# Optimization experiments

Measured on AMD Instinct MI355X. Metric: run time of the kernel, lower is better.

The kernel has to match this reference:

```python
import jax, jax.numpy as jnp
import numpy as np
import math

B, T, C = 2, 2048, 1024
H = 16
D = C // H  # 64


def setup_inputs() -> dict:
    key = jax.random.key(0)
    ks = jax.random.split(key, 12)
    s = 1.0 / math.sqrt(C)
    inp = {
        "q": jax.random.normal(ks[0], (B, T, C), dtype=jnp.float32),
        "k": jax.random.normal(ks[1], (B, T, C), dtype=jnp.float32),
        "v": jax.random.normal(ks[2], (B, T, C), dtype=jnp.float32),
        # causal mask, broadcastable to [B, H, T, T]; 0 -> masked
        "mask": jnp.tril(jnp.ones((T, T), dtype=jnp.int32))[None, None, :, :],
        "Wq": jax.random.normal(ks[3], (C, C), dtype=jnp.float32) * s,
        "bq": jnp.zeros((C,), dtype=jnp.float32),
        "Wk": jax.random.normal(ks[4], (C, C), dtype=jnp.float32) * s,
        "bk": jnp.zeros((C,), dtype=jnp.float32),
        "Wv": jax.random.normal(ks[5], (C, C), dtype=jnp.float32) * s,
        "bv": jnp.zeros((C,), dtype=jnp.float32),
        "Wo": jax.random.normal(ks[6], (C, C), dtype=jnp.float32) * s,
        "bo": jnp.zeros((C,), dtype=jnp.float32),
    }
    return inp


def reference(q, k, v, mask, Wq, bq, Wk, bk, Wv, bv, Wo, bo):
    # Linear projections (torch Linear: x @ W.T + b), split into heads -> [B,H,T,D]
    qh = (q @ Wq.T + bq).reshape(B, T, H, D).transpose(0, 2, 1, 3)
    kh = (k @ Wk.T + bk).reshape(B, T, H, D).transpose(0, 2, 1, 3)
    vh = (v @ Wv.T + bv).reshape(B, T, H, D).transpose(0, 2, 1, 3)
    # scaled dot-product attention with full [B,H,T,T] scores (faithful to source)
    scores = jnp.einsum("bhqd,bhkd->bhqk", qh, kh) / math.sqrt(D)
    scores = jnp.where(mask == 0, -jnp.inf, scores)
    attn = jax.nn.softmax(scores, axis=-1)  # dropout = identity (eval mode)
    out = jnp.einsum("bhqk,bhkd->bhqd", attn, vh)
    out = out.transpose(0, 2, 1, 3).reshape(B, T, C)
    return out @ Wo.T + bo
```

## Files before the change

kernel.cpp:

```cpp
#include <hip/hip_runtime.h>
#include <hip/hip_bf16.h>
#include <cstdint>
#include <cstddef>

#define B_ 2
#define T_ 2048
#define C_ 1024
#define H_ 16
#define D_ 64

typedef unsigned short u16;
typedef unsigned int u32;

typedef __bf16 bf16x8 __attribute__((ext_vector_type(8)));
typedef float f32x4 __attribute__((ext_vector_type(4)));

union BFQ {
    uint4 q;
    bf16x8 v;
    u16 s[8];
};

__device__ __forceinline__ u16 f2bf(float f) {
    union { float f; u32 u; } x;
    x.f = f;
    u32 u = x.u;
    return (u16)((u + 0x7FFFu + ((u >> 16) & 1u)) >> 16);
}

__device__ __forceinline__ void gl_lds16(const u16* g, u16* l) {
    __builtin_amdgcn_global_load_lds(
        (const __attribute__((address_space(1))) u32*)g,
        (__attribute__((address_space(3))) u32*)l, 16, 0, 0);
}

__global__ void cvt3_kernel(const float* __restrict__ i0, const float* __restrict__ i1,
                            const float* __restrict__ i2, u16* __restrict__ o0,
                            u16* __restrict__ o1, u16* __restrict__ o2, int n4) {
    const float* in = blockIdx.z == 0 ? i0 : (blockIdx.z == 1 ? i1 : i2);
    u16* out = blockIdx.z == 0 ? o0 : (blockIdx.z == 1 ? o1 : o2);
    int i = blockIdx.x * blockDim.x + threadIdx.x;
    int stride = gridDim.x * blockDim.x;
    for (; i < n4; i += stride) {
        float4 f = reinterpret_cast<const float4*>(in)[i];
        ushort4 o;
        o.x = f2bf(f.x);
        o.y = f2bf(f.y);
        o.z = f2bf(f.z);
        o.w = f2bf(f.w);
        reinterpret_cast<ushort4*>(out)[i] = o;
    }
}

__global__ void cvt4_kernel(const float* __restrict__ i0, const float* __restrict__ i1,
                            const float* __restrict__ i2, const float* __restrict__ i3,
                            u16* __restrict__ o0, u16* __restrict__ o1,
                            u16* __restrict__ o2, u16* __restrict__ o3, int n4) {
    int z = blockIdx.z;
    const float* in = z == 0 ? i0 : (z == 1 ? i1 : (z == 2 ? i2 : i3));
    u16* out = z == 0 ? o0 : (z == 1 ? o1 : (z == 2 ? o2 : o3));
    int i = blockIdx.x * blockDim.x + threadIdx.x;
    int stride = gridDim.x * blockDim.x;
    for (; i < n4; i += stride) {
        float4 f = reinterpret_cast<const float4*>(in)[i];
        ushort4 o;
        o.x = f2bf(f.x);
        o.y = f2bf(f.y);
        o.z = f2bf(f.z);
        o.w = f2bf(f.w);
        reinterpret_cast<ushort4*>(out)[i] = o;
    }
}

template <int OUT_BF16>
__device__ __forceinline__ void gemm_body(const u16* __restrict__ A,
                                          const u16* __restrict__ Bw,
                                          const float* __restrict__ bias,
                                          void* __restrict__ Cout,
                                          int M, int N, int K) {
    __shared__ u16 As[2][128 * 64];
    __shared__ u16 Bs[2][64 * 64];

    const int tid = threadIdx.x;
    const int lane = tid & 63;
    const int wave = tid >> 6;
    const int wm = wave >> 1, wn = wave & 1;
    const int g = lane >> 4, r = lane & 15;
    const int m0 = blockIdx.y * 128, n0 = blockIdx.x * 64;

    f32x4 acc[4][2] = {};

    const int lrow = lane >> 3;
    const int lcolS = ((lane & 7) ^ (lane >> 3)) * 8;
    const u16* Abase = A + (size_t)(m0 + lrow) * K + lcolS;
    const u16* Bbase = Bw + (size_t)(n0 + lrow) * K + lcolS;

#pragma unroll
    for (int c = 0; c < 4; ++c) {
        int ca = 4 * wave + c;
        gl_lds16(Abase + (size_t)(8 * ca) * K, As[0] + ca * 512);
    }
#pragma unroll
    for (int c = 0; c < 2; ++c) {
        int cb = 2 * wave + c;
        gl_lds16(Bbase + (size_t)(8 * cb) * K, Bs[0] + cb * 512);
    }
    __syncthreads();

    int cur = 0;
    for (int k0 = 0; k0 < K; k0 += 64) {
        if (k0 + 64 < K) {
#pragma unroll
            for (int c = 0; c < 4; ++c) {
                int ca = 4 * wave + c;
                gl_lds16(Abase + (size_t)(8 * ca) * K + k0 + 64, As[cur ^ 1] + ca * 512);
            }
#pragma unroll
            for (int c = 0; c < 2; ++c) {
                int cb = 2 * wave + c;
                gl_lds16(Bbase + (size_t)(8 * cb) * K + k0 + 64, Bs[cur ^ 1] + cb * 512);
            }
        }

#pragma unroll
        for (int kk = 0; kk < 2; ++kk) {
            bf16x8 af[4], bfv[2];
#pragma unroll
            for (int mt = 0; mt < 4; ++mt) {
                int row = wm * 64 + mt * 16 + r;
                BFQ u;
                u.q = *(const uint4*)(As[cur] + row * 64 + (((kk * 4 + g) ^ (r & 7)) * 8));
                af[mt] = u.v;
            }
#pragma unroll
            for (int nt = 0; nt < 2; ++nt) {
                int row = wn * 32 + nt * 16 + r;
                BFQ u;
                u.q = *(const uint4*)(Bs[cur] + row * 64 + (((kk * 4 + g) ^ (r & 7)) * 8));
                bfv[nt] = u.v;
            }
            __builtin_amdgcn_s_setprio(1);
#pragma unroll
            for (int mt = 0; mt < 4; ++mt)
#pragma unroll
                for (int nt = 0; nt < 2; ++nt)
                    acc[mt][nt] = __builtin_amdgcn_mfma_f32_16x16x32_bf16(af[mt], bfv[nt], acc[mt][nt], 0, 0, 0);
            __builtin_amdgcn_s_setprio(0);
        }
        __syncthreads();
        cur ^= 1;
    }

#pragma unroll
    for (int mt = 0; mt < 4; ++mt) {
#pragma unroll
        for (int nt = 0; nt < 2; ++nt) {
            int n = n0 + wn * 32 + nt * 16 + r;
            float bv = bias[n];
#pragma unroll
            for (int j = 0; j < 4; ++j) {
                int m = m0 + wm * 64 + mt * 16 + g * 4 + j;
                float val = acc[mt][nt][j] + bv;
                if (OUT_BF16)
                    ((u16*)Cout)[(size_t)m * N + n] = f2bf(val);
                else
                    ((float*)Cout)[(size_t)m * N + n] = val;
            }
        }
    }
}

__global__ __launch_bounds__(256, 2) void gemm3_kernel(
    const u16* __restrict__ A0, const u16* __restrict__ A1, const u16* __restrict__ A2,
    const u16* __restrict__ W0, const u16* __restrict__ W1, const u16* __restrict__ W2,
    const float* __restrict__ b0, const float* __restrict__ b1, const float* __restrict__ b2,
    u16* __restrict__ C0, u16* __restrict__ C1, u16* __restrict__ C2,
    int M, int N, int K) {
    int z = blockIdx.z;
    const u16* A = z == 0 ? A0 : (z == 1 ? A1 : A2);
    const u16* W = z == 0 ? W0 : (z == 1 ? W1 : W2);
    const float* bias = z == 0 ? b0 : (z == 1 ? b1 : b2);
    u16* C = z == 0 ? C0 : (z == 1 ? C1 : C2);
    gemm_body<1>(A, W, bias, C, M, N, K);
}

__global__ __launch_bounds__(256, 2) void gemm_f32_kernel(const u16* __restrict__ A,
                                                          const u16* __restrict__ W,
                                                          const float* __restrict__ bias,
                                                          float* __restrict__ C,
                                                          int M, int N, int K) {
    gemm_body<0>(A, W, bias, C, M, N, K);
}


__device__ __forceinline__ void softmax_step(f32x4* s, int domask, int kv0, int qrow0,
                                             int g, int r, float* m_run, float* l_run,
                                             f32x4* o_acc, u16* pl) {
    float sv[4][4];
#pragma unroll
    for (int nt = 0; nt < 4; ++nt) {
#pragma unroll
        for (int j = 0; j < 4; ++j) {
            float x = s[nt][j] * 0.125f;
            if (domask) {
                int kg = kv0 + nt * 16 + r;
                int qg = qrow0 + g * 4 + j;
                x = (kg <= qg) ? x : -1e30f;
            }
            sv[nt][j] = x;
        }
    }
    float rm[4];
#pragma unroll
    for (int j = 0; j < 4; ++j) {
        float m = fmaxf(fmaxf(sv[0][j], sv[1][j]), fmaxf(sv[2][j], sv[3][j]));
        m = fmaxf(m, __shfl_xor(m, 1));
        m = fmaxf(m, __shfl_xor(m, 2));
        m = fmaxf(m, __shfl_xor(m, 4));
        m = fmaxf(m, __shfl_xor(m, 8));
        rm[j] = m;
    }
    float grow = fmaxf(fmaxf(rm[0] - m_run[0], rm[1] - m_run[1]),
                       fmaxf(rm[2] - m_run[2], rm[3] - m_run[3]));
    float pout[4][4];
    float rs[4];
    if (__all(grow <= 8.0f)) {
#pragma unroll
        for (int j = 0; j < 4; ++j) {
            float mref = m_run[j];
            float p0 = __expf(sv[0][j] - mref);
            float p1 = __expf(sv[1][j] - mref);
            float p2 = __expf(sv[2][j] - mref);
            float p3 = __expf(sv[3][j] - mref);
            pout[0][j] = p0; pout[1][j] = p1; pout[2][j] = p2; pout[3][j] = p3;
            rs[j] = (p0 + p1) + (p2 + p3);
        }
    } else {
#pragma unroll
        for (int j = 0; j < 4; ++j) {
            float mnew = fmaxf(m_run[j], rm[j]);
            float fac = __expf(m_run[j] - mnew);
            float p0 = __expf(sv[0][j] - mnew);
            float p1 = __expf(sv[1][j] - mnew);
            float p2 = __expf(sv[2][j] - mnew);
            float p3 = __expf(sv[3][j] - mnew);
            pout[0][j] = p0; pout[1][j] = p1; pout[2][j] = p2; pout[3][j] = p3;
            rs[j] = (p0 + p1) + (p2 + p3);
            l_run[j] *= fac;
            m_run[j] = mnew;
#pragma unroll
            for (int nt = 0; nt < 4; ++nt) o_acc[nt][j] *= fac;
        }
    }
#pragma unroll
    for (int j = 0; j < 4; ++j) {
        float t = rs[j];
        t += __shfl_xor(t, 1);
        t += __shfl_xor(t, 2);
        t += __shfl_xor(t, 4);
        t += __shfl_xor(t, 8);
        l_run[j] += t;
        int q = g * 4 + j;
        int sw = (q & 7) << 3;
        pl[(q * 64 + 0 * 16 + r) ^ sw] = f2bf(pout[0][j]);
        pl[(q * 64 + 1 * 16 + r) ^ sw] = f2bf(pout[1][j]);
        pl[(q * 64 + 2 * 16 + r) ^ sw] = f2bf(pout[2][j]);
        pl[(q * 64 + 3 * 16 + r) ^ sw] = f2bf(pout[3][j]);
    }
}

__global__ __launch_bounds__(256, 2) void attn_kernel(const u16* __restrict__ Qp,
                                                      const u16* __restrict__ Kp,
                                                      const u16* __restrict__ Vp,
                                                      u16* __restrict__ Op) {
    __shared__ u16 Vt[64 * 64];
    __shared__ u16 Pl[4][2][16 * 64];

    const int tid = threadIdx.x, lane = tid & 63, wave = tid >> 6;
    const int g = lane >> 4, r = lane & 15;
    const int bh = blockIdx.y, b = bh >> 4, h = bh & 15;
    const int i = blockIdx.x;
    const int qA0 = i * 64;
    const int qB0 = (31 - i) * 64;

    const u16* Qbh = Qp + ((size_t)b * T_) * C_ + h * 64;
    const u16* Kbh = Kp + ((size_t)b * T_) * C_ + h * 64;
    const u16* Vbh = Vp + ((size_t)b * T_) * C_ + h * 64;
    u16* Obh = Op + ((size_t)b * T_) * C_ + h * 64;

    bf16x8 aqA[2], aqB[2];
    {
        const u16* qa = Qbh + (size_t)(qA0 + wave * 16 + r) * C_ + g * 8;
        const u16* qb = Qbh + (size_t)(qB0 + wave * 16 + r) * C_ + g * 8;
        BFQ u0, u1, u2, u3;
        u0.q = *(const uint4*)(qa);
        u1.q = *(const uint4*)(qa + 32);
        u2.q = *(const uint4*)(qb);
        u3.q = *(const uint4*)(qb + 32);
        aqA[0] = u0.v; aqA[1] = u1.v;
        aqB[0] = u2.v; aqB[1] = u3.v;
    }

    float mA[4], lA[4], mB[4], lB[4];
    f32x4 oA[4] = {}, oB[4] = {};
#pragma unroll
    for (int j = 0; j < 4; ++j) {
        mA[j] = -1e30f; lA[j] = 0.f;
        mB[j] = -1e30f; lB[j] = 0.f;
    }

    const int vp = tid & 31;
    const int vd0 = (tid >> 5) * 8;

    BFQ kf[2][4];
#pragma unroll
    for (int kk = 0; kk < 2; ++kk)
#pragma unroll
        for (int nt = 0; nt < 4; ++nt)
            kf[kk][nt].q = *(const uint4*)(Kbh + (size_t)(nt * 16 + r) * C_ + kk * 32 + g * 8);
    BFQ va, vb;
    {
        const u16* vr0 = Vbh + (size_t)(2 * vp) * C_ + vd0;
        va.q = *(const uint4*)(vr0);
        vb.q = *(const uint4*)(vr0 + C_);
    }

    for (int kv0 = 0; kv0 <= qB0; kv0 += 64) {
        const int actA = (kv0 <= qA0);

        __builtin_amdgcn_s_barrier();

#pragma unroll
        for (int ii = 0; ii < 8; ++ii) {
            int d = vd0 + ii;
            u32 pr = (u32)va.s[ii] | ((u32)vb.s[ii] << 16);
            *(u32*)&Vt[(d * 64 + 2 * vp) ^ ((d & 7) << 3)] = pr;
        }

        f32x4 sB[4] = {}, sA[4] = {};
        __builtin_amdgcn_s_setprio(1);
#pragma unroll
        for (int kk = 0; kk < 2; ++kk)
#pragma unroll
            for (int nt = 0; nt < 4; ++nt)
                sB[nt] = __builtin_amdgcn_mfma_f32_16x16x32_bf16(aqB[kk], kf[kk][nt].v, sB[nt], 0, 0, 0);
        if (actA) {
#pragma unroll
            for (int kk = 0; kk < 2; ++kk)
#pragma unroll
                for (int nt = 0; nt < 4; ++nt)
                    sA[nt] = __builtin_amdgcn_mfma_f32_16x16x32_bf16(aqA[kk], kf[kk][nt].v, sA[nt], 0, 0, 0);
        }
        __builtin_amdgcn_s_setprio(0);

        if (kv0 + 64 <= qB0) {
            const u16* kn = Kbh + (size_t)(kv0 + 64) * C_;
#pragma unroll
            for (int kk = 0; kk < 2; ++kk)
#pragma unroll
                for (int nt = 0; nt < 4; ++nt)
                    kf[kk][nt].q = *(const uint4*)(kn + (size_t)(nt * 16 + r) * C_ + kk * 32 + g * 8);
            const u16* vr0 = Vbh + (size_t)(kv0 + 64 + 2 * vp) * C_ + vd0;
            va.q = *(const uint4*)(vr0);
            vb.q = *(const uint4*)(vr0 + C_);
        }

        softmax_step(sB, kv0 == qB0, kv0, qB0 + wave * 16, g, r, mB, lB, oB, Pl[wave][0]);
        if (actA)
            softmax_step(sA, kv0 == qA0, kv0, qA0 + wave * 16, g, r, mA, lA, oA, Pl[wave][1]);

        asm volatile("s_waitcnt lgkmcnt(0)" ::: "memory");
        __builtin_amdgcn_s_barrier();

        bf16x8 vf[2][4];
#pragma unroll
        for (int kk = 0; kk < 2; ++kk)
#pragma unroll
            for (int nt = 0; nt < 4; ++nt) {
                int d = nt * 16 + r;
                BFQ u;
                u.q = *(const uint4*)&Vt[(d * 64 + kk * 32 + g * 8) ^ ((d & 7) << 3)];
                vf[kk][nt] = u.v;
            }

        __builtin_amdgcn_s_setprio(1);
#pragma unroll
        for (int kk = 0; kk < 2; ++kk) {
            BFQ ua;
            ua.q = *(const uint4*)&Pl[wave][0][(r * 64 + kk * 32 + g * 8) ^ ((r & 7) << 3)];
#pragma unroll
            for (int nt = 0; nt < 4; ++nt)
                oB[nt] = __builtin_amdgcn_mfma_f32_16x16x32_bf16(ua.v, vf[kk][nt], oB[nt], 0, 0, 0);
        }
        if (actA) {
#pragma unroll
            for (int kk = 0; kk < 2; ++kk) {
                BFQ ua;
                ua.q = *(const uint4*)&Pl[wave][1][(r * 64 + kk * 32 + g * 8) ^ ((r & 7) << 3)];
#pragma unroll
                for (int nt = 0; nt < 4; ++nt)
                    oA[nt] = __builtin_amdgcn_mfma_f32_16x16x32_bf16(ua.v, vf[kk][nt], oA[nt], 0, 0, 0);
            }
        }
        __builtin_amdgcn_s_setprio(0);
    }

#pragma unroll
    for (int nt = 0; nt < 4; ++nt) {
#pragma unroll
        for (int j = 0; j < 4; ++j) {
            int qgB = qB0 + wave * 16 + g * 4 + j;
            Obh[(size_t)qgB * C_ + nt * 16 + r] = f2bf(oB[nt][j] / lB[j]);
            int qgA = qA0 + wave * 16 + g * 4 + j;
            Obh[(size_t)qgA * C_ + nt * 16 + r] = f2bf(oA[nt][j] / lA[j]);
        }
    }
}

extern "C" void kernel_launch(void* const* d_in, const int* in_sizes, int n_in,
                              void* d_out, int out_size, void* d_ws, size_t ws_size,
                              hipStream_t stream) {
    const float* q = (const float*)d_in[0];
    const float* k = (const float*)d_in[1];
    const float* v = (const float*)d_in[2];
    const float* Wq = (const float*)d_in[4];
    const float* bq = (const float*)d_in[5];
    const float* Wk = (const float*)d_in[6];
    const float* bk = (const float*)d_in[7];
    const float* Wv = (const float*)d_in[8];
    const float* bv = (const float*)d_in[9];
    const float* Wo = (const float*)d_in[10];
    const float* bo = (const float*)d_in[11];

    const size_t NTC = (size_t)B_ * T_ * C_;
    const size_t NW = (size_t)C_ * C_;

    char* ws = (char*)d_ws;
    size_t off = 0;
    u16* qb = (u16*)(ws + off);  off += NTC * 2;
    u16* kb = (u16*)(ws + off);  off += NTC * 2;
    u16* vb = (u16*)(ws + off);  off += NTC * 2;
    u16* Wqb = (u16*)(ws + off); off += NW * 2;
    u16* Wkb = (u16*)(ws + off); off += NW * 2;
    u16* Wvb = (u16*)(ws + off); off += NW * 2;
    u16* Wob = (u16*)(ws + off); off += NW * 2;
    u16* Qp = (u16*)(ws + off);  off += NTC * 2;
    u16* Kp = (u16*)(ws + off);  off += NTC * 2;
    u16* Vp = (u16*)(ws + off);  off += NTC * 2;
    u16* AOb = (u16*)(ws + off); off += NTC * 2;

    cvt3_kernel<<<dim3(512, 1, 3), 256, 0, stream>>>(q, k, v, qb, kb, vb, (int)(NTC / 4));
    cvt4_kernel<<<dim3(128, 1, 4), 256, 0, stream>>>(Wq, Wk, Wv, Wo, Wqb, Wkb, Wvb, Wob, (int)(NW / 4));

    const int M = B_ * T_;
    dim3 g3(C_ / 64, M / 128, 3);
    gemm3_kernel<<<g3, 256, 0, stream>>>(qb, kb, vb, Wqb, Wkb, Wvb, bq, bk, bv,
                                         Qp, Kp, Vp, M, C_, C_);

    dim3 agrid(16, B_ * H_);
    attn_kernel<<<agrid, 256, 0, stream>>>(Qp, Kp, Vp, AOb);

    dim3 g1(C_ / 64, M / 128, 1);
    gemm_f32_kernel<<<g1, 256, 0, stream>>>(AOb, Wob, bo, (float*)d_out, M, C_, C_);
}
```

Before: 157.7 us.

## Split attention tiles across 8 waves and fold softmax scale into Q with exp2

The attention block grows to 512 threads. Waves 0-3 handle the late (long) query tile and waves 4-7 handle the early tile, so each wave keeps one set of accumulators instead of two, which lowers register pressure and adds parallelism. Q is pre-scaled by log2(e)/sqrt(D) so softmax can use the hardware exp2 directly, with the deferred-rescale threshold adjusted to match. The GEMM launch bounds are raised to 3 blocks per CU, and float-to-bf16 conversion now uses the native cast. The risks are that the early-tile waves sit idle once their tile is done yet still join the barriers, and that rounding the scaled Q to bf16 adds a little error.

Measured after the change: 196.0 us. 1.24x slower.

```diff
diff --git a/kernel.cpp b/kernel.cpp
--- a/kernel.cpp
+++ b/kernel.cpp
@@ -15,17 +15,25 @@
 typedef __bf16 bf16x8 __attribute__((ext_vector_type(8)));
 typedef float f32x4 __attribute__((ext_vector_type(4)));
 
+#define QSCALE 0.18033688011112042f
+#define DEFER_THR 11.5f
+
 union BFQ {
     uint4 q;
     bf16x8 v;
     u16 s[8];
 };
 
+__device__ __forceinline__ float bf2f(u16 s) {
+    union { u32 u; float f; } x;
+    x.u = ((u32)s) << 16;
+    return x.f;
+}
+
 __device__ __forceinline__ u16 f2bf(float f) {
-    union { float f; u32 u; } x;
-    x.f = f;
-    u32 u = x.u;
-    return (u16)((u + 0x7FFFu + ((u >> 16) & 1u)) >> 16);
+    union { __bf16 h; u16 u; } c;
+    c.h = (__bf16)f;
+    return c.u;
 }
 
 __device__ __forceinline__ void gl_lds16(const u16* g, u16* l) {
@@ -170,7 +178,7 @@
     }
 }
 
-__global__ __launch_bounds__(256, 2) void gemm3_kernel(
+__global__ __launch_bounds__(256, 3) void gemm3_kernel(
     const u16* __restrict__ A0, const u16* __restrict__ A1, const u16* __restrict__ A2,
     const u16* __restrict__ W0, const u16* __restrict__ W1, const u16* __restrict__ W2,
     const float* __restrict__ b0, const float* __restrict__ b1, const float* __restrict__ b2,
@@ -184,7 +192,7 @@
     gemm_body<1>(A, W, bias, C, M, N, K);
 }
 
-__global__ __launch_bounds__(256, 2) void gemm_f32_kernel(const u16* __restrict__ A,
+__global__ __launch_bounds__(256, 3) void gemm_f32_kernel(const u16* __restrict__ A,
                                                           const u16* __restrict__ W,
                                                           const float* __restrict__ bias,
                                                           float* __restrict__ C,
@@ -201,7 +209,7 @@
     for (int nt = 0; nt < 4; ++nt) {
 #pragma unroll
         for (int j = 0; j < 4; ++j) {
-            float x = s[nt][j] * 0.125f;
+            float x = s[nt][j];
             if (domask) {
                 int kg = kv0 + nt * 16 + r;
                 int qg = qrow0 + g * 4 + j;
@@ -224,14 +232,14 @@
                        fmaxf(rm[2] - m_run[2], rm[3] - m_run[3]));
     float pout[4][4];
     float rs[4];
-    if (__all(grow <= 8.0f)) {
+    if (__all(grow <= DEFER_THR)) {
 #pragma unroll
         for (int j = 0; j < 4; ++j) {
             float mref = m_run[j];
-            float p0 = __expf(sv[0][j] - mref);
-            float p1 = __expf(sv[1][j] - mref);
-            float p2 = __expf(sv[2][j] - mref);
-            float p3 = __expf(sv[3][j] - mref);
+            float p0 = __builtin_amdgcn_exp2f(sv[0][j] - mref);
+            float p1 = __builtin_amdgcn_exp2f(sv[1][j] - mref);
+            float p2 = __builtin_amdgcn_exp2f(sv[2][j] - mref);
+            float p3 = __builtin_amdgcn_exp2f(sv[3][j] - mref);
             pout[0][j] = p0; pout[1][j] = p1; pout[2][j] = p2; pout[3][j] = p3;
             rs[j] = (p0 + p1) + (p2 + p3);
         }
@@ -239,11 +247,11 @@
 #pragma unroll
         for (int j = 0; j < 4; ++j) {
             float mnew = fmaxf(m_run[j], rm[j]);
-            float fac = __expf(m_run[j] - mnew);
-            float p0 = __expf(sv[0][j] - mnew);
-            float p1 = __expf(sv[1][j] - mnew);
-            float p2 = __expf(sv[2][j] - mnew);
-            float p3 = __expf(sv[3][j] - mnew);
+            float fac = __builtin_amdgcn_exp2f(m_run[j] - mnew);
+            float p0 = __builtin_amdgcn_exp2f(sv[0][j] - mnew);
+            float p1 = __builtin_amdgcn_exp2f(sv[1][j] - mnew);
+            float p2 = __builtin_amdgcn_exp2f(sv[2][j] - mnew);
+            float p3 = __builtin_amdgcn_exp2f(sv[3][j] - mnew);
             pout[0][j] = p0; pout[1][j] = p1; pout[2][j] = p2; pout[3][j] = p3;
             rs[j] = (p0 + p1) + (p2 + p3);
             l_run[j] *= fac;
@@ -269,48 +277,54 @@
     }
 }
 
-__global__ __launch_bounds__(256, 2) void attn_kernel(const u16* __restrict__ Qp,
+__global__ __launch_bounds__(512, 2) void attn_kernel(const u16* __restrict__ Qp,
                                                       const u16* __restrict__ Kp,
                                                       const u16* __restrict__ Vp,
                                                       u16* __restrict__ Op) {
     __shared__ u16 Vt[64 * 64];
-    __shared__ u16 Pl[4][2][16 * 64];
+    __shared__ u16 Pl[8][16 * 64];
 
     const int tid = threadIdx.x, lane = tid & 63, wave = tid >> 6;
     const int g = lane >> 4, r = lane & 15;
+    const int tileSel = wave >> 2;
+    const int wsub = wave & 3;
     const int bh = blockIdx.y, b = bh >> 4, h = bh & 15;
     const int i = blockIdx.x;
-    const int qA0 = i * 64;
     const int qB0 = (31 - i) * 64;
+    const int q0 = tileSel ? i * 64 : qB0;
 
     const u16* Qbh = Qp + ((size_t)b * T_) * C_ + h * 64;
     const u16* Kbh = Kp + ((size_t)b * T_) * C_ + h * 64;
     const u16* Vbh = Vp + ((size_t)b * T_) * C_ + h * 64;
     u16* Obh = Op + ((size_t)b * T_) * C_ + h * 64;
 
-    bf16x8 aqA[2], aqB[2];
+    bf16x8 aq[2];
     {
-        const u16* qa = Qbh + (size_t)(qA0 + wave * 16 + r) * C_ + g * 8;
-        const u16* qb = Qbh + (size_t)(qB0 + wave * 16 + r) * C_ + g * 8;
-        BFQ u0, u1, u2, u3;
+        const u16* qa = Qbh + (size_t)(q0 + wsub * 16 + r) * C_ + g * 8;
+        BFQ u0, u1;
         u0.q = *(const uint4*)(qa);
         u1.q = *(const uint4*)(qa + 32);
-        u2.q = *(const uint4*)(qb);
-        u3.q = *(const uint4*)(qb + 32);
-        aqA[0] = u0.v; aqA[1] = u1.v;
-        aqB[0] = u2.v; aqB[1] = u3.v;
-    }
-
-    float mA[4], lA[4], mB[4], lB[4];
-    f32x4 oA[4] = {}, oB[4] = {};
+#pragma unroll
+        for (int e = 0; e < 8; ++e) {
+            u0.s[e] = f2bf(bf2f(u0.s[e]) * QSCALE);
+            u1.s[e] = f2bf(bf2f(u1.s[e]) * QSCALE);
+        }
+        aq[0] = u0.v;
+        aq[1] = u1.v;
+    }
+
+    float m_run[4], l_run[4];
+    f32x4 o_acc[4] = {};
 #pragma unroll
     for (int j = 0; j < 4; ++j) {
-        mA[j] = -1e30f; lA[j] = 0.f;
-        mB[j] = -1e30f; lB[j] = 0.f;
-    }
-
-    const int vp = tid & 31;
-    const int vd0 = (tid >> 5) * 8;
+        m_run[j] = -1e30f;
+        l_run[j] = 0.f;
+    }
+
+    const int stager = tileSel;
+    const int st = tid & 255;
+    const int vp = st & 31;
+    const int vd0 = (st >> 5) * 8;
 
     BFQ kf[2][4];
 #pragma unroll
@@ -319,100 +333,87 @@
         for (int nt = 0; nt < 4; ++nt)
             kf[kk][nt].q = *(const uint4*)(Kbh + (size_t)(nt * 16 + r) * C_ + kk * 32 + g * 8);
     BFQ va, vb;
-    {
+    if (stager) {
         const u16* vr0 = Vbh + (size_t)(2 * vp) * C_ + vd0;
         va.q = *(const uint4*)(vr0);
         vb.q = *(const uint4*)(vr0 + C_);
     }
 
     for (int kv0 = 0; kv0 <= qB0; kv0 += 64) {
-        const int actA = (kv0 <= qA0);
+        const int act = (kv0 <= q0);
 
         __builtin_amdgcn_s_barrier();
 
-#pragma unroll
-        for (int ii = 0; ii < 8; ++ii) {
-            int d = vd0 + ii;
-            u32 pr = (u32)va.s[ii] | ((u32)vb.s[ii] << 16);
-            *(u32*)&Vt[(d * 64 + 2 * vp) ^ ((d & 7) << 3)] = pr;
-        }
-
-        f32x4 sB[4] = {}, sA[4] = {};
-        __builtin_amdgcn_s_setprio(1);
-#pragma unroll
-        for (int kk = 0; kk < 2; ++kk)
-#pragma unroll
-            for (int nt = 0; nt < 4; ++nt)
-                sB[nt] = __builtin_amdgcn_mfma_f32_16x16x32_bf16(aqB[kk], kf[kk][nt].v, sB[nt], 0, 0, 0);
-        if (actA) {
+        if (stager) {
+#pragma unroll
+            for (int ii = 0; ii < 8; ++ii) {
+                int d = vd0 + ii;
+                u32 pr = (u32)va.s[ii] | ((u32)vb.s[ii] << 16);
+                *(u32*)&Vt[(d * 64 + 2 * vp) ^ ((d & 7) << 3)] = pr;
+            }
+        }
+
+        f32x4 s[4] = {};
+        if (act) {
+            __builtin_amdgcn_s_setprio(1);
 #pragma unroll
             for (int kk = 0; kk < 2; ++kk)
 #pragma unroll
                 for (int nt = 0; nt < 4; ++nt)
-                    sA[nt] = __builtin_amdgcn_mfma_f32_16x16x32_bf16(aqA[kk], kf[kk][nt].v, sA[nt], 0, 0, 0);
-        }
-        __builtin_amdgcn_s_setprio(0);
-
-        if (kv0 + 64 <= qB0) {
+                    s[nt] = __builtin_amdgcn_mfma_f32_16x16x32_bf16(aq[kk], kf[kk][nt].v, s[nt], 0, 0, 0);
+            __builtin_amdgcn_s_setprio(0);
+        }
+
+        if (kv0 + 64 <= q0) {
             const u16* kn = Kbh + (size_t)(kv0 + 64) * C_;
 #pragma unroll
             for (int kk = 0; kk < 2; ++kk)
 #pragma unroll
                 for (int nt = 0; nt < 4; ++nt)
                     kf[kk][nt].q = *(const uint4*)(kn + (size_t)(nt * 16 + r) * C_ + kk * 32 + g * 8);
+        }
+        if (stager && kv0 + 64 <= qB0) {
             const u16* vr0 = Vbh + (size_t)(kv0 + 64 + 2 * vp) * C_ + vd0;
             va.q = *(const uint4*)(vr0);
             vb.q = *(const uint4*)(vr0 + C_);
         }
 
-        softmax_step(sB, kv0 == qB0, kv0, qB0 + wave * 16, g, r, mB, lB, oB, Pl[wave][0]);
-        if (actA)
-            softmax_step(sA, kv0 == qA0, kv0, qA0 + wave * 16, g, r, mA, lA, oA, Pl[wave][1]);
+        if (act)
+            softmax_step(s, kv0 == q0, kv0, q0 + wsub * 16, g, r, m_run, l_run, o_acc, Pl[wave]);
 
         asm volatile("s_waitcnt lgkmcnt(0)" ::: "memory");
         __builtin_amdgcn_s_barrier();
 
-        bf16x8 vf[2][4];
-#pragma unroll
-        for (int kk = 0; kk < 2; ++kk)
-#pragma unroll
-            for (int nt = 0; nt < 4; ++nt) {
-                int d = nt * 16 + r;
-                BFQ u;
-                u.q = *(const uint4*)&Vt[(d * 64 + kk * 32 + g * 8) ^ ((d & 7) << 3)];
-                vf[kk][nt] = u.v;
-            }
-
-        __builtin_amdgcn_s_setprio(1);
-#pragma unroll
-        for (int kk = 0; kk < 2; ++kk) {
-            BFQ ua;
-            ua.q = *(const uint4*)&Pl[wave][0][(r * 64 + kk * 32 + g * 8) ^ ((r & 7) << 3)];
-#pragma unroll
-            for (int nt = 0; nt < 4; ++nt)
-                oB[nt] = __builtin_amdgcn_mfma_f32_16x16x32_bf16(ua.v, vf[kk][nt], oB[nt], 0, 0, 0);
-        }
-        if (actA) {
+        if (act) {
+            bf16x8 vf[2][4];
+#pragma unroll
+            for (int kk = 0; kk < 2; ++kk)
+#pragma unroll
+                for (int nt = 0; nt < 4; ++nt) {
+                    int d = nt * 16 + r;
+                    BFQ u;
+                    u.q = *(const uint4*)&Vt[(d * 64 + kk * 32 + g * 8) ^ ((d & 7) << 3)];
+                    vf[kk][nt] = u.v;
+                }
+            __builtin_amdgcn_s_setprio(1);
 #pragma unroll
             for (int kk = 0; kk < 2; ++kk) {
                 BFQ ua;
-                ua.q = *(const uint4*)&Pl[wave][1][(r * 64 + kk * 32 + g * 8) ^ ((r & 7) << 3)];
+                ua.q = *(const uint4*)&Pl[wave][(r * 64 + kk * 32 + g * 8) ^ ((r & 7) << 3)];
 #pragma unroll
                 for (int nt = 0; nt < 4; ++nt)
-                    oA[nt] = __builtin_amdgcn_mfma_f32_16x16x32_bf16(ua.v, vf[kk][nt], oA[nt], 0, 0, 0);
-            }
-        }
-        __builtin_amdgcn_s_setprio(0);
+                    o_acc[nt] = __builtin_amdgcn_mfma_f32_16x16x32_bf16(ua.v, vf[kk][nt], o_acc[nt], 0, 0, 0);
+            }
+            __builtin_amdgcn_s_setprio(0);
+        }
     }
 
 #pragma unroll
     for (int nt = 0; nt < 4; ++nt) {
 #pragma unroll
         for (int j = 0; j < 4; ++j) {
-            int qgB = qB0 + wave * 16 + g * 4 + j;
-            Obh[(size_t)qgB * C_ + nt * 16 + r] = f2bf(oB[nt][j] / lB[j]);
-            int qgA = qA0 + wave * 16 + g * 4 + j;
-            Obh[(size_t)qgA * C_ + nt * 16 + r] = f2bf(oA[nt][j] / lA[j]);
+            int qg = q0 + wsub * 16 + g * 4 + j;
+            Obh[(size_t)qg * C_ + nt * 16 + r] = f2bf(o_acc[nt][j] / l_run[j]);
         }
     }
 }
@@ -458,7 +459,7 @@
                                          Qp, Kp, Vp, M, C_, C_);
 
     dim3 agrid(16, B_ * H_);
-    attn_kernel<<<agrid, 256, 0, stream>>>(Qp, Kp, Vp, AOb);
+    attn_kernel<<<agrid, 512, 0, stream>>>(Qp, Kp, Vp, AOb);
 
     dim3 g1(C_ / 64, M / 128, 1);
     gemm_f32_kernel<<<g1, 256, 0, stream>>>(AOb, Wob, bo, (float*)d_out, M, C_, C_);
```

## Split attention KV loop across two blocks and merge partial softmax results

Applied to the files above, without the earlier changes.

The attention grid doubles along z. Each block handles alternating 64-key tiles and writes unnormalized bf16 partial outputs plus running max and sum, and a new merge kernel combines the two halves with log-sum-exp weights. The goal is more parallelism from 512 attention blocks instead of 256. Q is also prescaled by log2(e)/sqrt(D) so the softmax can use exp2 directly, with a looser deferred-rescale threshold, and the GEMM launch bounds move to 3 blocks per CU. In exchange the unnormalized partials are rounded to bf16, and the merge kernel adds a launch plus extra global traffic.

Measured after the change: 168.7 us. +7.0%, slower.

```diff
diff --git a/kernel.cpp b/kernel.cpp
--- a/kernel.cpp
+++ b/kernel.cpp
@@ -15,17 +15,25 @@
 typedef __bf16 bf16x8 __attribute__((ext_vector_type(8)));
 typedef float f32x4 __attribute__((ext_vector_type(4)));
 
+#define QSCALE 0.18033688011112042f
+#define DEFER_THR 11.5f
+
 union BFQ {
     uint4 q;
     bf16x8 v;
     u16 s[8];
 };
 
+__device__ __forceinline__ float bf2f(u16 s) {
+    union { u32 u; float f; } x;
+    x.u = ((u32)s) << 16;
+    return x.f;
+}
+
 __device__ __forceinline__ u16 f2bf(float f) {
-    union { float f; u32 u; } x;
-    x.f = f;
-    u32 u = x.u;
-    return (u16)((u + 0x7FFFu + ((u >> 16) & 1u)) >> 16);
+    union { __bf16 h; u16 u; } c;
+    c.h = (__bf16)f;
+    return c.u;
 }
 
 __device__ __forceinline__ void gl_lds16(const u16* g, u16* l) {
@@ -170,7 +178,7 @@
     }
 }
 
-__global__ __launch_bounds__(256, 2) void gemm3_kernel(
+__global__ __launch_bounds__(256, 3) void gemm3_kernel(
     const u16* __restrict__ A0, const u16* __restrict__ A1, const u16* __restrict__ A2,
     const u16* __restrict__ W0, const u16* __restrict__ W1, const u16* __restrict__ W2,
     const float* __restrict__ b0, const float* __restrict__ b1, const float* __restrict__ b2,
@@ -184,7 +192,7 @@
     gemm_body<1>(A, W, bias, C, M, N, K);
 }
 
-__global__ __launch_bounds__(256, 2) void gemm_f32_kernel(const u16* __restrict__ A,
+__global__ __launch_bounds__(256, 3) void gemm_f32_kernel(const u16* __restrict__ A,
                                                           const u16* __restrict__ W,
                                                           const float* __restrict__ bias,
                                                           float* __restrict__ C,
@@ -201,7 +209,7 @@
     for (int nt = 0; nt < 4; ++nt) {
 #pragma unroll
         for (int j = 0; j < 4; ++j) {
-            float x = s[nt][j] * 0.125f;
+            float x = s[nt][j];
             if (domask) {
                 int kg = kv0 + nt * 16 + r;
                 int qg = qrow0 + g * 4 + j;
@@ -224,14 +232,14 @@
                        fmaxf(rm[2] - m_run[2], rm[3] - m_run[3]));
     float pout[4][4];
     float rs[4];
-    if (__all(grow <= 8.0f)) {
+    if (__all(grow <= DEFER_THR)) {
 #pragma unroll
         for (int j = 0; j < 4; ++j) {
             float mref = m_run[j];
-            float p0 = __expf(sv[0][j] - mref);
-            float p1 = __expf(sv[1][j] - mref);
-            float p2 = __expf(sv[2][j] - mref);
-            float p3 = __expf(sv[3][j] - mref);
+            float p0 = __builtin_amdgcn_exp2f(sv[0][j] - mref);
+            float p1 = __builtin_amdgcn_exp2f(sv[1][j] - mref);
+            float p2 = __builtin_amdgcn_exp2f(sv[2][j] - mref);
+            float p3 = __builtin_amdgcn_exp2f(sv[3][j] - mref);
             pout[0][j] = p0; pout[1][j] = p1; pout[2][j] = p2; pout[3][j] = p3;
             rs[j] = (p0 + p1) + (p2 + p3);
         }
@@ -239,11 +247,11 @@
 #pragma unroll
         for (int j = 0; j < 4; ++j) {
             float mnew = fmaxf(m_run[j], rm[j]);
-            float fac = __expf(m_run[j] - mnew);
-            float p0 = __expf(sv[0][j] - mnew);
-            float p1 = __expf(sv[1][j] - mnew);
-            float p2 = __expf(sv[2][j] - mnew);
-            float p3 = __expf(sv[3][j] - mnew);
+            float fac = __builtin_amdgcn_exp2f(m_run[j] - mnew);
+            float p0 = __builtin_amdgcn_exp2f(sv[0][j] - mnew);
+            float p1 = __builtin_amdgcn_exp2f(sv[1][j] - mnew);
+            float p2 = __builtin_amdgcn_exp2f(sv[2][j] - mnew);
+            float p3 = __builtin_amdgcn_exp2f(sv[3][j] - mnew);
             pout[0][j] = p0; pout[1][j] = p1; pout[2][j] = p2; pout[3][j] = p3;
             rs[j] = (p0 + p1) + (p2 + p3);
             l_run[j] *= fac;
@@ -272,7 +280,9 @@
 __global__ __launch_bounds__(256, 2) void attn_kernel(const u16* __restrict__ Qp,
                                                       const u16* __restrict__ Kp,
                                                       const u16* __restrict__ Vp,
-                                                      u16* __restrict__ Op) {
+                                                      u16* __restrict__ OP0,
+                                                      u16* __restrict__ OP1,
+                                                      float* __restrict__ ML) {
     __shared__ u16 Vt[64 * 64];
     __shared__ u16 Pl[4][2][16 * 64];
 
@@ -280,13 +290,13 @@
     const int g = lane >> 4, r = lane & 15;
     const int bh = blockIdx.y, b = bh >> 4, h = bh & 15;
     const int i = blockIdx.x;
+    const int z = blockIdx.z;
     const int qA0 = i * 64;
     const int qB0 = (31 - i) * 64;
 
     const u16* Qbh = Qp + ((size_t)b * T_) * C_ + h * 64;
     const u16* Kbh = Kp + ((size_t)b * T_) * C_ + h * 64;
     const u16* Vbh = Vp + ((size_t)b * T_) * C_ + h * 64;
-    u16* Obh = Op + ((size_t)b * T_) * C_ + h * 64;
 
     bf16x8 aqA[2], aqB[2];
     {
@@ -297,6 +307,13 @@
         u1.q = *(const uint4*)(qa + 32);
         u2.q = *(const uint4*)(qb);
         u3.q = *(const uint4*)(qb + 32);
+#pragma unroll
+        for (int e = 0; e < 8; ++e) {
+            u0.s[e] = f2bf(bf2f(u0.s[e]) * QSCALE);
+            u1.s[e] = f2bf(bf2f(u1.s[e]) * QSCALE);
+            u2.s[e] = f2bf(bf2f(u2.s[e]) * QSCALE);
+            u3.s[e] = f2bf(bf2f(u3.s[e]) * QSCALE);
+        }
         aqA[0] = u0.v; aqA[1] = u1.v;
         aqB[0] = u2.v; aqB[1] = u3.v;
     }
@@ -317,15 +334,15 @@
     for (int kk = 0; kk < 2; ++kk)
 #pragma unroll
         for (int nt = 0; nt < 4; ++nt)
-            kf[kk][nt].q = *(const uint4*)(Kbh + (size_t)(nt * 16 + r) * C_ + kk * 32 + g * 8);
+            kf[kk][nt].q = *(const uint4*)(Kbh + (size_t)(z * 64 + nt * 16 + r) * C_ + kk * 32 + g * 8);
     BFQ va, vb;
     {
-        const u16* vr0 = Vbh + (size_t)(2 * vp) * C_ + vd0;
+        const u16* vr0 = Vbh + (size_t)(z * 64 + 2 * vp) * C_ + vd0;
         va.q = *(const uint4*)(vr0);
         vb.q = *(const uint4*)(vr0 + C_);
     }
 
-    for (int kv0 = 0; kv0 <= qB0; kv0 += 64) {
+    for (int kv0 = z * 64; kv0 <= qB0; kv0 += 128) {
         const int actA = (kv0 <= qA0);
 
         __builtin_amdgcn_s_barrier();
@@ -353,14 +370,14 @@
         }
         __builtin_amdgcn_s_setprio(0);
 
-        if (kv0 + 64 <= qB0) {
-            const u16* kn = Kbh + (size_t)(kv0 + 64) * C_;
+        if (kv0 + 128 <= qB0) {
+            const u16* kn = Kbh + (size_t)(kv0 + 128) * C_;
 #pragma unroll
             for (int kk = 0; kk < 2; ++kk)
 #pragma unroll
                 for (int nt = 0; nt < 4; ++nt)
                     kf[kk][nt].q = *(const uint4*)(kn + (size_t)(nt * 16 + r) * C_ + kk * 32 + g * 8);
-            const u16* vr0 = Vbh + (size_t)(kv0 + 64 + 2 * vp) * C_ + vd0;
+            const u16* vr0 = Vbh + (size_t)(kv0 + 128 + 2 * vp) * C_ + vd0;
             va.q = *(const uint4*)(vr0);
             vb.q = *(const uint4*)(vr0 + C_);
         }
@@ -405,16 +422,55 @@
         __builtin_amdgcn_s_setprio(0);
     }
 
+    u16* OPz = z ? OP1 : OP0;
+    u16* Obh = OPz + ((size_t)b * T_) * C_ + h * 64;
+    float* MLz = ML + (((size_t)z * 32 + bh) * T_) * 2;
 #pragma unroll
     for (int nt = 0; nt < 4; ++nt) {
 #pragma unroll
         for (int j = 0; j < 4; ++j) {
             int qgB = qB0 + wave * 16 + g * 4 + j;
-            Obh[(size_t)qgB * C_ + nt * 16 + r] = f2bf(oB[nt][j] / lB[j]);
+            Obh[(size_t)qgB * C_ + nt * 16 + r] = f2bf(oB[nt][j]);
             int qgA = qA0 + wave * 16 + g * 4 + j;
-            Obh[(size_t)qgA * C_ + nt * 16 + r] = f2bf(oA[nt][j] / lA[j]);
-        }
-    }
+            Obh[(size_t)qgA * C_ + nt * 16 + r] = f2bf(oA[nt][j]);
+        }
+    }
+    if (r == 0) {
+#pragma unroll
+        for (int j = 0; j < 4; ++j) {
+            int qgB = qB0 + wave * 16 + g * 4 + j;
+            MLz[qgB * 2 + 0] = mB[j];
+            MLz[qgB * 2 + 1] = lB[j];
+            int qgA = qA0 + wave * 16 + g * 4 + j;
+            MLz[qgA * 2 + 0] = mA[j];
+            MLz[qgA * 2 + 1] = lA[j];
+        }
+    }
+}
+
+__global__ void merge_kernel(const u16* __restrict__ O0, const u16* __restrict__ O1,
+                             const float* __restrict__ ML, u16* __restrict__ Out) {
+    int idx = blockIdx.x * blockDim.x + threadIdx.x;
+    size_t base = (size_t)idx * 8;
+    int h = (int)((base >> 6) & 15);
+    int q = (int)((base >> 10) & (T_ - 1));
+    int b = (int)(base >> 21);
+    int bh = b * 16 + h;
+    const float* ml0 = ML + (((size_t)0 * 32 + bh) * T_ + q) * 2;
+    const float* ml1 = ML + (((size_t)1 * 32 + bh) * T_ + q) * 2;
+    float m0 = ml0[0], l0 = ml0[1];
+    float m1 = ml1[0], l1 = ml1[1];
+    float mM = fmaxf(m0, m1);
+    float w0 = __builtin_amdgcn_exp2f(m0 - mM);
+    float w1 = __builtin_amdgcn_exp2f(m1 - mM);
+    float inv = 1.0f / (l0 * w0 + l1 * w1);
+    BFQ a, c, o;
+    a.q = *(const uint4*)(O0 + base);
+    c.q = *(const uint4*)(O1 + base);
+#pragma unroll
+    for (int e = 0; e < 8; ++e)
+        o.s[e] = f2bf((bf2f(a.s[e]) * w0 + bf2f(c.s[e]) * w1) * inv);
+    *(uint4*)(Out + base) = o.q;
 }
 
 extern "C" void kernel_launch(void* const* d_in, const int* in_sizes, int n_in,
@@ -449,6 +505,10 @@
     u16* Vp = (u16*)(ws + off);  off += NTC * 2;
     u16* AOb = (u16*)(ws + off); off += NTC * 2;
 
+    u16* OP0 = qb;
+    u16* OP1 = kb;
+    float* ML = (float*)vb;
+
     cvt3_kernel<<<dim3(512, 1, 3), 256, 0, stream>>>(q, k, v, qb, kb, vb, (int)(NTC / 4));
     cvt4_kernel<<<dim3(128, 1, 4), 256, 0, stream>>>(Wq, Wk, Wv, Wo, Wqb, Wkb, Wvb, Wob, (int)(NW / 4));
 
@@ -457,8 +517,10 @@
     gemm3_kernel<<<g3, 256, 0, stream>>>(qb, kb, vb, Wqb, Wkb, Wvb, bq, bk, bv,
                                          Qp, Kp, Vp, M, C_, C_);
 
-    dim3 agrid(16, B_ * H_);
-    attn_kernel<<<agrid, 256, 0, stream>>>(Qp, Kp, Vp, AOb);
+    dim3 agrid(16, B_ * H_, 2);
+    attn_kernel<<<agrid, 256, 0, stream>>>(Qp, Kp, Vp, OP0, OP1, ML);
+
+    merge_kernel<<<(int)(NTC / 8 / 256), 256, 0, stream>>>(OP0, OP1, ML, AOb);
 
     dim3 g1(C_ / 64, M / 128, 1);
     gemm_f32_kernel<<<g1, 256, 0, stream>>>(AOb, Wob, bo, (float*)d_out, M, C_, C_);
```
